# Kernel tuning notes

Hardware: AMD Instinct MI355X
Metric: run time of the kernel (lower is better)

Reference implementation:

```python
import jax, jax.numpy as jnp
import numpy as np

N = 100000          # nodes
E = 1600000         # edges (avg degree 16)
F_IN = 128          # num_node_features
H = 128             # hidden_channels
C = 8               # num_classes
EPS = 1e-5          # batchnorm eps
SLOPE = 0.01        # leaky_relu negative slope


def setup_inputs() -> dict:
    key = jax.random.key(0)
    ks = jax.random.split(key, 12)
    s = 0.05
    inp = {
        "node_feat": jax.random.normal(ks[0], (N, F_IN), jnp.float32),
        "src": jax.random.randint(ks[1], (E,), 0, N, dtype=jnp.int32),
        "dst": jax.random.randint(ks[2], (E,), 0, N, dtype=jnp.int32),
        # conv1 / conv2 (GraphConv weights + bias)
        "W1": jax.random.normal(ks[3], (F_IN, H), jnp.float32) * s,
        "b1": jnp.zeros((H,), jnp.float32),
        "W2": jax.random.normal(ks[4], (H, H), jnp.float32) * s,
        "b2": jnp.zeros((H,), jnp.float32),
        # batchnorm affine params
        "gamma1": jnp.ones((H,), jnp.float32),
        "beta1": jnp.zeros((H,), jnp.float32),
        "gamma2": jnp.ones((H,), jnp.float32),
        "beta2": jnp.zeros((H,), jnp.float32),
        # convnode1 / convnode2
        "Wn1": jax.random.normal(ks[5], (H, H), jnp.float32) * s,
        "bn1": jnp.zeros((H,), jnp.float32),
        "Wn2": jax.random.normal(ks[6], (H, H), jnp.float32) * s,
        "bn2": jnp.zeros((H,), jnp.float32),
        # node classifier
        "Wc": jax.random.normal(ks[7], (H, C), jnp.float32) * s,
        "bc": jnp.zeros((C,), jnp.float32),
    }
    return inp


def _deg_inv_sqrt(idx):
    # clamp(deg, min=1) ** -0.5, as in DGL GraphConv norm='both'
    deg = jax.ops.segment_sum(jnp.ones((E,), jnp.float32), idx, num_segments=N)
    return jnp.clip(deg, 1.0, None) ** -0.5


def _gconv(x, src, dst, W, b, out_norm, in_norm):
    # DGL GraphConv, norm='both': gather src-normalized feats, scatter-add to dst,
    # normalize by in-degree, then dense transform.
    msg = (x * out_norm[:, None])[src]                    # [E, d] gather
    agg = jax.ops.segment_sum(msg, dst, num_segments=N)   # [N, d] scatter-add
    return (agg * in_norm[:, None]) @ W + b


def _bn(x, gamma, beta):
    # training-mode BatchNorm1d: batch mean / biased var
    mean = jnp.mean(x, axis=0)
    var = jnp.var(x, axis=0)
    return (x - mean) * jax.lax.rsqrt(var + EPS) * gamma + beta


def _lrelu(x):
    return jnp.where(x >= 0, x, SLOPE * x)


def reference(node_feat, src, dst, W1, b1, W2, b2, gamma1, beta1, gamma2, beta2,
              Wn1, bn1, Wn2, bn2, Wc, bc):
    out_norm = _deg_inv_sqrt(src)   # src out-degree norm
    in_norm = _deg_inv_sqrt(dst)    # dst in-degree norm

    h = _gconv(node_feat, src, dst, W1, b1, out_norm, in_norm)
    h = _lrelu(_bn(h, gamma1, beta1))
    h = _gconv(h, src, dst, W2, b2, out_norm, in_norm)
    h = _lrelu(_bn(h, gamma2, beta2))

    hn = _lrelu(_gconv(h, src, dst, Wn1, bn1, out_norm, in_norm))
    hn = _lrelu(_gconv(hn, src, dst, Wn2, bn2, out_norm, in_norm))

    return hn @ Wc + bc   # [N, C]
```

## Files before the change

kernel.cpp:

```cpp
#include <hip/hip_runtime.h>
#include <math.h>

#define HN 128
#define NC 8
#define EPSV 1e-5f
#define SLOPEV 0.01f

typedef __attribute__((ext_vector_type(4))) float f32x4;
typedef __attribute__((ext_vector_type(8))) short bf16x8;

__device__ __forceinline__ uint bf16rne(float f) {
    uint u = __float_as_uint(f);
    return (u + 0x7fffu + ((u >> 16) & 1u)) >> 16;
}

__global__ __launch_bounds__(256) void rank_kernel(
        const int* __restrict__ src, const int* __restrict__ dst,
        int* __restrict__ degO, int* __restrict__ cntI,
        int* __restrict__ rnk, int E) {
    int base = blockIdx.x * 1024 + threadIdx.x;
    int s[4], d[4], r[4];
    #pragma unroll
    for (int k = 0; k < 4; k++) {
        int e = base + k * 256;
        if (e < E) { s[k] = src[e]; d[k] = dst[e]; }
    }
    #pragma unroll
    for (int k = 0; k < 4; k++) {
        int e = base + k * 256;
        if (e < E) atomicAdd(&degO[s[k]], 1);
    }
    #pragma unroll
    for (int k = 0; k < 4; k++) {
        int e = base + k * 256;
        if (e < E) r[k] = atomicAdd(&cntI[d[k]], 1);
    }
    #pragma unroll
    for (int k = 0; k < 4; k++) {
        int e = base + k * 256;
        if (e < E) rnk[e] = r[k];
    }
}

__global__ __launch_bounds__(256) void scan_partial(const int* __restrict__ degI,
                                                    int* __restrict__ blockSums, int n) {
    __shared__ int sS[256];
    int tid = threadIdx.x;
    int base = blockIdx.x * 1024 + tid * 4;
    int s = 0;
    #pragma unroll
    for (int j = 0; j < 4; j++) {
        int idx = base + j;
        s += (idx < n) ? degI[idx] : 0;
    }
    sS[tid] = s;
    __syncthreads();
    for (int off = 128; off; off >>= 1) {
        if (tid < off) sS[tid] += sS[tid + off];
        __syncthreads();
    }
    if (tid == 0) blockSums[blockIdx.x] = sS[0];
}

__global__ __launch_bounds__(1024) void scan_blocksums(int* __restrict__ blockSums, int nb) {
    __shared__ int sS[1024];
    int tid = threadIdx.x;
    int v = (tid < nb) ? blockSums[tid] : 0;
    sS[tid] = v;
    __syncthreads();
    for (int off = 1; off < 1024; off <<= 1) {
        int t = (tid >= off) ? sS[tid - off] : 0;
        __syncthreads();
        sS[tid] += t;
        __syncthreads();
    }
    if (tid < nb) blockSums[tid] = sS[tid] - v;
}

__global__ __launch_bounds__(256) void scan_final(const int* __restrict__ degI,
                                                  const int* __restrict__ degO,
                                                  const int* __restrict__ blockSums,
                                                  int* __restrict__ row_ptr,
                                                  float* __restrict__ onorm,
                                                  float* __restrict__ inorm, int n, int E) {
    __shared__ int sS[256];
    int tid = threadIdx.x;
    int base = blockIdx.x * 1024 + tid * 4;
    int v[4];
    int tot = 0;
    #pragma unroll
    for (int j = 0; j < 4; j++) {
        int idx = base + j;
        int vv = (idx < n) ? degI[idx] : 0;
        v[j] = tot;
        tot += vv;
    }
    sS[tid] = tot;
    __syncthreads();
    for (int off = 1; off < 256; off <<= 1) {
        int t = (tid >= off) ? sS[tid - off] : 0;
        __syncthreads();
        sS[tid] += t;
        __syncthreads();
    }
    int tb = blockSums[blockIdx.x] + sS[tid] - tot;
    #pragma unroll
    for (int j = 0; j < 4; j++) {
        int idx = base + j;
        if (idx < n) {
            row_ptr[idx] = tb + v[j];
            float a = (float)degO[idx]; if (a < 1.f) a = 1.f;
            float b = (float)degI[idx]; if (b < 1.f) b = 1.f;
            onorm[idx] = rsqrtf(a);
            inorm[idx] = rsqrtf(b);
        }
    }
    if (blockIdx.x == 0 && tid == 0) row_ptr[n] = E;
}

__global__ __launch_bounds__(256) void scatter_kernel(
        const int* __restrict__ src, const int* __restrict__ dst,
        const int* __restrict__ rnk, const int* __restrict__ row_ptr,
        int* __restrict__ srcs, int E) {
    int base = blockIdx.x * 1024 + threadIdx.x;
    int s[4], d[4], r[4], rp[4];
    #pragma unroll
    for (int k = 0; k < 4; k++) {
        int e = base + k * 256;
        if (e < E) { d[k] = dst[e]; r[k] = rnk[e]; s[k] = src[e]; }
    }
    #pragma unroll
    for (int k = 0; k < 4; k++) {
        int e = base + k * 256;
        if (e < E) rp[k] = row_ptr[d[k]];
    }
    #pragma unroll
    for (int k = 0; k < 4; k++) {
        int e = base + k * 256;
        if (e < E) srcs[rp[k] + r[k]] = s[k];
    }
}

__global__ __launch_bounds__(256) void wprep_kernel(
        const float* __restrict__ W1, const float* __restrict__ W2,
        const float* __restrict__ W3, const float* __restrict__ W4,
        ushort* __restrict__ WTh, ushort* __restrict__ WTl) {
    int i = blockIdx.x * blockDim.x + threadIdx.x;
    int l = i >> 14, r = i & 16383;
    int k = r >> 7, nn = r & 127;
    const float* W = (l == 0) ? W1 : (l == 1) ? W2 : (l == 2) ? W3 : W4;
    float w = W[k * HN + nn];
    uint hi = bf16rne(w);
    float fhi = __uint_as_float(hi << 16);
    uint lo = bf16rne(w - fhi);
    WTh[(size_t)l * 16384 + nn * HN + k] = (ushort)hi;
    WTl[(size_t)l * 16384 + nn * HN + k] = (ushort)lo;
}

__global__ __launch_bounds__(256) void pack_kernel(
        const float* __restrict__ in, const float* __restrict__ onorm,
        ushort* __restrict__ out, int total4) {
    int i = blockIdx.x * blockDim.x + threadIdx.x;
    if (i >= total4) return;
    float w = onorm[i >> 5];
    float4 v = ((const float4*)in)[i];
    ushort4 o = make_ushort4((ushort)bf16rne(v.x * w), (ushort)bf16rne(v.y * w),
                             (ushort)bf16rne(v.z * w), (ushort)bf16rne(v.w * w));
    *(ushort4*)(out + (size_t)i * 4) = o;
}

__global__ __launch_bounds__(256) void bnpack_kernel(
        const float* __restrict__ in, ushort* __restrict__ out,
        const float* __restrict__ scale, const float* __restrict__ shift,
        const float* __restrict__ onorm, int total4) {
    int i = blockIdx.x * blockDim.x + threadIdx.x;
    if (i >= total4) return;
    int cp = (i & 31) << 2;
    float w = onorm[i >> 5];
    float4 v = ((const float4*)in)[i];
    float4 s = *(const float4*)(scale + cp);
    float4 t = *(const float4*)(shift + cp);
    float h0 = fmaf(v.x, s.x, t.x); h0 = (h0 >= 0.f) ? h0 : SLOPEV * h0;
    float h1 = fmaf(v.y, s.y, t.y); h1 = (h1 >= 0.f) ? h1 : SLOPEV * h1;
    float h2 = fmaf(v.z, s.z, t.z); h2 = (h2 >= 0.f) ? h2 : SLOPEV * h2;
    float h3 = fmaf(v.w, s.w, t.w); h3 = (h3 >= 0.f) ? h3 : SLOPEV * h3;
    ushort4 o = make_ushort4((ushort)bf16rne(h0 * w), (ushort)bf16rne(h1 * w),
                             (ushort)bf16rne(h2 * w), (ushort)bf16rne(h3 * w));
    *(ushort4*)(out + (size_t)i * 4) = o;
}

__global__ __launch_bounds__(256) void agg_kernel(
        const uint* __restrict__ xb, uint* __restrict__ out,
        const int* __restrict__ srcs, const int* __restrict__ row_ptr,
        const float* __restrict__ inorm, int n) {
    int node = blockIdx.x * 4 + (threadIdx.x >> 6);
    if (node >= n) return;
    int lane = threadIdx.x & 63;
    int rp0 = row_ptr[node], rp1 = row_ptr[node + 1];
    float accx = 0.f, accy = 0.f;
    int j = rp0;
    for (; j + 3 < rp1; j += 4) {
        int s0 = srcs[j], s1 = srcs[j + 1], s2 = srcs[j + 2], s3 = srcs[j + 3];
        uint u0 = xb[(size_t)s0 * 64 + lane];
        uint u1 = xb[(size_t)s1 * 64 + lane];
        uint u2 = xb[(size_t)s2 * 64 + lane];
        uint u3 = xb[(size_t)s3 * 64 + lane];
        accx += __uint_as_float(u0 << 16) + __uint_as_float(u1 << 16)
              + __uint_as_float(u2 << 16) + __uint_as_float(u3 << 16);
        accy += __uint_as_float(u0 & 0xffff0000u) + __uint_as_float(u1 & 0xffff0000u)
              + __uint_as_float(u2 & 0xffff0000u) + __uint_as_float(u3 & 0xffff0000u);
    }
    for (; j < rp1; j++) {
        uint u0 = xb[(size_t)srcs[j] * 64 + lane];
        accx += __uint_as_float(u0 << 16);
        accy += __uint_as_float(u0 & 0xffff0000u);
    }
    float wi = inorm[node];
    uint o = bf16rne(accx * wi) | (bf16rne(accy * wi) << 16);
    out[(size_t)node * 64 + lane] = o;
}

template<int DO_STATS, int DO_LRELU, int DO_PACK>
__global__ __launch_bounds__(512) void gemm_mfma(
        const ushort* __restrict__ A, const uint4* __restrict__ WTh4,
        const uint4* __restrict__ WTl4, const float* __restrict__ bias,
        void* __restrict__ outv, float* __restrict__ colsum, float* __restrict__ colsq,
        const float* __restrict__ onorm, int n) {
    __shared__ uint4 sW[4096];
    int tid = threadIdx.x;
    #pragma unroll
    for (int it = 0; it < 4; it++) {
        int j = it * 512 + tid;
        int nrow = j >> 4, c = j & 15;
        int sidx = nrow * 16 + (c ^ (nrow & 15));
        sW[sidx] = WTh4[j];
        sW[2048 + sidx] = WTl4[j];
    }
    __syncthreads();

    int wave = tid >> 6, lane = tid & 63;
    int l15 = lane & 15, quad = lane >> 4;
    int rbase = blockIdx.x * 128 + wave * 16;
    int arow = rbase + l15; if (arow > n - 1) arow = n - 1;

    bf16x8 af[4];
    #pragma unroll
    for (int kc = 0; kc < 4; kc++)
        af[kc] = *(const bf16x8*)(A + (size_t)arow * HN + kc * 32 + quad * 8);

    f32x4 acc[8];
    #pragma unroll
    for (int t = 0; t < 8; t++) acc[t] = (f32x4){0.f, 0.f, 0.f, 0.f};

    #pragma unroll
    for (int t = 0; t < 8; t++) {
        int nn = t * 16 + l15;
        int base = nn * 16, sw = nn & 15;
        #pragma unroll
        for (int kc = 0; kc < 4; kc++) {
            int c = kc * 4 + quad;
            bf16x8 bh = *(const bf16x8*)&sW[base + (c ^ sw)];
            acc[t] = __builtin_amdgcn_mfma_f32_16x16x32_bf16(af[kc], bh, acc[t], 0, 0, 0);
        }
        #pragma unroll
        for (int kc = 0; kc < 4; kc++) {
            int c = kc * 4 + quad;
            bf16x8 bl = *(const bf16x8*)&sW[2048 + base + (c ^ sw)];
            acc[t] = __builtin_amdgcn_mfma_f32_16x16x32_bf16(af[kc], bl, acc[t], 0, 0, 0);
        }
    }

    float sarr[8], qarr[8];
    #pragma unroll
    for (int t = 0; t < 8; t++) {
        int col = t * 16 + l15;
        float bv = bias[col];
        float s = 0.f, q = 0.f;
        #pragma unroll
        for (int i = 0; i < 4; i++) {
            int row = rbase + quad * 4 + i;
            float v = acc[t][i] + bv;
            if (DO_LRELU) v = (v >= 0.f) ? v : SLOPEV * v;
            if (row < n) {
                if (DO_PACK) {
                    ((ushort*)outv)[(size_t)row * HN + col] = (ushort)bf16rne(v * onorm[row]);
                } else {
                    ((float*)outv)[(size_t)row * HN + col] = v;
                }
                if (DO_STATS) { s += v; q += v * v; }
            }
        }
        if (DO_STATS) {
            s += __shfl_xor(s, 16); q += __shfl_xor(q, 16);
            s += __shfl_xor(s, 32); q += __shfl_xor(q, 32);
        }
        sarr[t] = s; qarr[t] = q;
    }

    if (DO_STATS) {
        __syncthreads();
        float* sSum = (float*)sW;
        float* sSq  = (float*)sW + 1024;
        if (quad == 0) {
            #pragma unroll
            for (int t = 0; t < 8; t++) {
                sSum[wave * 128 + t * 16 + l15] = sarr[t];
                sSq [wave * 128 + t * 16 + l15] = qarr[t];
            }
        }
        __syncthreads();
        if (tid < 128) {
            float s = 0.f, q = 0.f;
            #pragma unroll
            for (int w = 0; w < 8; w++) { s += sSum[w * 128 + tid]; q += sSq[w * 128 + tid]; }
            atomicAdd(&colsum[tid], s);
            atomicAdd(&colsq[tid], q);
        }
    }
}

__global__ void bn_finalize(const float* __restrict__ colsum, const float* __restrict__ colsq,
                            const float* __restrict__ gamma, const float* __restrict__ beta,
                            float* __restrict__ scale, float* __restrict__ shift, int n) {
    int c = threadIdx.x;
    if (c < HN) {
        float inv = 1.f / (float)n;
        float mean = colsum[c] * inv;
        float var = colsq[c] * inv - mean * mean;
        if (var < 0.f) var = 0.f;
        float s = gamma[c] * rsqrtf(var + EPSV);
        scale[c] = s;
        shift[c] = beta[c] - mean * s;
    }
}

__global__ __launch_bounds__(256) void classifier_kernel(
        const float* __restrict__ A, const float* __restrict__ Wc,
        const float* __restrict__ bc, float* __restrict__ out, int n) {
    __shared__ float sW[HN * NC];
    __shared__ float sA[32 * 132];
    int tid = threadIdx.x;
    for (int i = tid; i < HN * NC; i += 256) sW[i] = Wc[i];
    int row0 = blockIdx.x * 32;
    for (int i = tid; i < 32 * 32; i += 256) {
        int r = i >> 5, c4 = (i & 31) << 2;
        float4 v = (row0 + r < n) ? *(const float4*)(A + (size_t)(row0 + r) * HN + c4)
                                  : make_float4(0.f, 0.f, 0.f, 0.f);
        *(float4*)&sA[r * 132 + c4] = v;
    }
    __syncthreads();
    int r = tid >> 3, c = tid & 7;
    float acc = 0.f;
    #pragma unroll 8
    for (int k = 0; k < HN; k++) acc = fmaf(sA[r * 132 + k], sW[k * NC + c], acc);
    int row = row0 + r;
    if (row < n) out[(size_t)row * NC + c] = acc + bc[c];
}

extern "C" void kernel_launch(void* const* d_in, const int* in_sizes, int n_in,
                              void* d_out, int out_size, void* d_ws, size_t ws_size,
                              hipStream_t stream) {
    const float* node_feat = (const float*)d_in[0];
    const int*   src    = (const int*)d_in[1];
    const int*   dst    = (const int*)d_in[2];
    const float* W1     = (const float*)d_in[3];
    const float* b1     = (const float*)d_in[4];
    const float* W2     = (const float*)d_in[5];
    const float* b2     = (const float*)d_in[6];
    const float* gamma1 = (const float*)d_in[7];
    const float* beta1  = (const float*)d_in[8];
    const float* gamma2 = (const float*)d_in[9];
    const float* beta2  = (const float*)d_in[10];
    const float* Wn1    = (const float*)d_in[11];
    const float* bn1    = (const float*)d_in[12];
    const float* Wn2    = (const float*)d_in[13];
    const float* bn2    = (const float*)d_in[14];
    const float* Wc     = (const float*)d_in[15];
    const float* bc     = (const float*)d_in[16];
    float* out = (float*)d_out;

    const int N = in_sizes[0] / HN;
    const int E = in_sizes[1];

    char* p = (char*)d_ws;
    float* bufA  = (float*)p; p += (size_t)N * HN * 4;
    float* bufB  = (float*)p; p += (size_t)N * HN * 4;
    float* onorm = (float*)p; p += (size_t)N * 4;
    float* inorm = (float*)p; p += (size_t)N * 4;
    float* scale = (float*)p; p += HN * 4;
    float* shift = (float*)p; p += HN * 4;
    char* zbase = p;
    float* cs1 = (float*)p; p += HN * 4;
    float* cq1 = (float*)p; p += HN * 4;
    float* cs2 = (float*)p; p += HN * 4;
    float* cq2 = (float*)p; p += HN * 4;
    int* degO = (int*)p; p += (size_t)N * 4;
    int* cntI = (int*)p; p += (size_t)N * 4;
    size_t zbytes = (size_t)(p - zbase);
    int* row_ptr = (int*)p; p += (size_t)(N + 4) * 4;
    int* blockSums = (int*)p; p += 1024 * 4;
    int* rnk     = (int*)p; p += (size_t)E * 4;
    int* srcs    = (int*)p; p += (size_t)E * 4;
    ushort* WTh  = (ushort*)p; p += 4 * 16384 * 2;
    ushort* WTl  = (ushort*)p; p += 4 * 16384 * 2;
    if ((size_t)(p - (char*)d_ws) > ws_size) return;

    hipMemsetAsync(zbase, 0, zbytes, stream);

    int gE4 = (E + 1023) / 1024;
    int nb = (N + 1023) / 1024;
    rank_kernel<<<gE4, 256, 0, stream>>>(src, dst, degO, cntI, rnk, E);
    scan_partial<<<nb, 256, 0, stream>>>(cntI, blockSums, N);
    scan_blocksums<<<1, 1024, 0, stream>>>(blockSums, nb);
    scan_final<<<nb, 256, 0, stream>>>(cntI, degO, blockSums, row_ptr, onorm, inorm, N, E);
    scatter_kernel<<<gE4, 256, 0, stream>>>(src, dst, rnk, row_ptr, srcs, E);
    wprep_kernel<<<256, 256, 0, stream>>>(W1, W2, Wn1, Wn2, WTh, WTl);

    int gAgg = (N + 3) / 4;
    int gGemm = (N + 127) / 128;
    int gApply = (N * 32 + 255) / 256;

    ushort* HbA = (ushort*)bufA;
    ushort* Abf = (ushort*)bufA + (size_t)N * HN;
    ushort* HbB = (ushort*)bufB;

    pack_kernel<<<gApply, 256, 0, stream>>>(node_feat, onorm, HbA, N * 32);
    agg_kernel<<<gAgg, 256, 0, stream>>>((const uint*)HbA, (uint*)Abf, srcs, row_ptr, inorm, N);
    gemm_mfma<1, 0, 0><<<gGemm, 512, 0, stream>>>(Abf, (const uint4*)WTh, (const uint4*)WTl,
                                                  b1, bufB, cs1, cq1, nullptr, N);
    bn_finalize<<<1, 128, 0, stream>>>(cs1, cq1, gamma1, beta1, scale, shift, N);
    bnpack_kernel<<<gApply, 256, 0, stream>>>(bufB, HbA, scale, shift, onorm, N * 32);

    agg_kernel<<<gAgg, 256, 0, stream>>>((const uint*)HbA, (uint*)Abf, srcs, row_ptr, inorm, N);
    gemm_mfma<1, 0, 0><<<gGemm, 512, 0, stream>>>(Abf, (const uint4*)(WTh + 16384),
                                                  (const uint4*)(WTl + 16384),
                                                  b2, bufB, cs2, cq2, nullptr, N);
    bn_finalize<<<1, 128, 0, stream>>>(cs2, cq2, gamma2, beta2, scale, shift, N);
    bnpack_kernel<<<gApply, 256, 0, stream>>>(bufB, HbA, scale, shift, onorm, N * 32);

    agg_kernel<<<gAgg, 256, 0, stream>>>((const uint*)HbA, (uint*)Abf, srcs, row_ptr, inorm, N);
    gemm_mfma<0, 1, 1><<<gGemm, 512, 0, stream>>>(Abf, (const uint4*)(WTh + 2 * 16384),
                                                  (const uint4*)(WTl + 2 * 16384),
                                                  bn1, HbB, nullptr, nullptr, onorm, N);

    agg_kernel<<<gAgg, 256, 0, stream>>>((const uint*)HbB, (uint*)Abf, srcs, row_ptr, inorm, N);
    gemm_mfma<0, 1, 0><<<gGemm, 512, 0, stream>>>(Abf, (const uint4*)(WTh + 3 * 16384),
                                                  (const uint4*)(WTl + 3 * 16384),
                                                  bn2, bufB, nullptr, nullptr, nullptr, N);
    classifier_kernel<<<(N + 31) / 32, 256, 0, stream>>>(bufB, Wc, bc, out, N);
}
```

Measured before the change: 757.6 us.

## Split bf16 feature buffers into four column slabs for cache-local aggregation

Feature buffers are stored as four 32-column slabs ([4][N][32] bf16) instead of row-major [N][128]. The aggregation kernel handles one slab per block range, and each wave processes four edges in parallel (16 lanes per edge), then combines the partial sums with cross-lane shuffles. Each slab is about 6.4 MB, so the random gathers for one slab should stay resident in L2/infinity cache instead of streaming the full 25.6 MB table. The cost is four passes over the CSR index arrays, 64-byte gathers in place of 256-byte row reads, and extra shuffle reductions; the GEMM A-load and the packed output store are adapted to the new layout.

```diff
diff --git a/kernel.cpp b/kernel.cpp
--- a/kernel.cpp
+++ b/kernel.cpp
@@ -159,65 +159,76 @@
 
 __global__ __launch_bounds__(256) void pack_kernel(
         const float* __restrict__ in, const float* __restrict__ onorm,
-        ushort* __restrict__ out, int total4) {
+        ushort* __restrict__ out, int nrows) {
     int i = blockIdx.x * blockDim.x + threadIdx.x;
-    if (i >= total4) return;
-    float w = onorm[i >> 5];
+    if (i >= nrows * 32) return;
+    int row = i >> 5, c4 = (i & 31) << 2;
+    float w = onorm[row];
     float4 v = ((const float4*)in)[i];
     ushort4 o = make_ushort4((ushort)bf16rne(v.x * w), (ushort)bf16rne(v.y * w),
                              (ushort)bf16rne(v.z * w), (ushort)bf16rne(v.w * w));
-    *(ushort4*)(out + (size_t)i * 4) = o;
+    int q = c4 >> 5, lc = c4 & 31;
+    *(ushort4*)(out + ((size_t)q * nrows + row) * 32 + lc) = o;
 }
 
 __global__ __launch_bounds__(256) void bnpack_kernel(
         const float* __restrict__ in, ushort* __restrict__ out,
         const float* __restrict__ scale, const float* __restrict__ shift,
-        const float* __restrict__ onorm, int total4) {
+        const float* __restrict__ onorm, int nrows) {
     int i = blockIdx.x * blockDim.x + threadIdx.x;
-    if (i >= total4) return;
-    int cp = (i & 31) << 2;
-    float w = onorm[i >> 5];
+    if (i >= nrows * 32) return;
+    int row = i >> 5, c4 = (i & 31) << 2;
+    float w = onorm[row];
     float4 v = ((const float4*)in)[i];
-    float4 s = *(const float4*)(scale + cp);
-    float4 t = *(const float4*)(shift + cp);
+    float4 s = *(const float4*)(scale + c4);
+    float4 t = *(const float4*)(shift + c4);
     float h0 = fmaf(v.x, s.x, t.x); h0 = (h0 >= 0.f) ? h0 : SLOPEV * h0;
     float h1 = fmaf(v.y, s.y, t.y); h1 = (h1 >= 0.f) ? h1 : SLOPEV * h1;
     float h2 = fmaf(v.z, s.z, t.z); h2 = (h2 >= 0.f) ? h2 : SLOPEV * h2;
     float h3 = fmaf(v.w, s.w, t.w); h3 = (h3 >= 0.f) ? h3 : SLOPEV * h3;
     ushort4 o = make_ushort4((ushort)bf16rne(h0 * w), (ushort)bf16rne(h1 * w),
                              (ushort)bf16rne(h2 * w), (ushort)bf16rne(h3 * w));
-    *(ushort4*)(out + (size_t)i * 4) = o;
+    int q = c4 >> 5, lc = c4 & 31;
+    *(ushort4*)(out + ((size_t)q * nrows + row) * 32 + lc) = o;
 }
 
 __global__ __launch_bounds__(256) void agg_kernel(
-        const uint* __restrict__ xb, uint* __restrict__ out,
+        const uint* __restrict__ xb, uint* __restrict__ outb,
         const int* __restrict__ srcs, const int* __restrict__ row_ptr,
-        const float* __restrict__ inorm, int n) {
-    int node = blockIdx.x * 4 + (threadIdx.x >> 6);
+        const float* __restrict__ inorm, int n, int nodeBlocks) {
+    int q = blockIdx.x / nodeBlocks;
+    int nb = blockIdx.x - q * nodeBlocks;
+    int node = nb * 4 + (threadIdx.x >> 6);
     if (node >= n) return;
     int lane = threadIdx.x & 63;
+    int g = lane >> 4, li = lane & 15;
+    const uint* Q = xb + (size_t)q * n * 16;
     int rp0 = row_ptr[node], rp1 = row_ptr[node + 1];
     float accx = 0.f, accy = 0.f;
-    int j = rp0;
-    for (; j + 3 < rp1; j += 4) {
-        int s0 = srcs[j], s1 = srcs[j + 1], s2 = srcs[j + 2], s3 = srcs[j + 3];
-        uint u0 = xb[(size_t)s0 * 64 + lane];
-        uint u1 = xb[(size_t)s1 * 64 + lane];
-        uint u2 = xb[(size_t)s2 * 64 + lane];
-        uint u3 = xb[(size_t)s3 * 64 + lane];
+    int j = rp0 + g;
+    for (; j + 12 < rp1; j += 16) {
+        int s0 = srcs[j], s1 = srcs[j + 4], s2 = srcs[j + 8], s3 = srcs[j + 12];
+        uint u0 = Q[(size_t)s0 * 16 + li];
+        uint u1 = Q[(size_t)s1 * 16 + li];
+        uint u2 = Q[(size_t)s2 * 16 + li];
+        uint u3 = Q[(size_t)s3 * 16 + li];
         accx += __uint_as_float(u0 << 16) + __uint_as_float(u1 << 16)
               + __uint_as_float(u2 << 16) + __uint_as_float(u3 << 16);
         accy += __uint_as_float(u0 & 0xffff0000u) + __uint_as_float(u1 & 0xffff0000u)
               + __uint_as_float(u2 & 0xffff0000u) + __uint_as_float(u3 & 0xffff0000u);
     }
-    for (; j < rp1; j++) {
-        uint u0 = xb[(size_t)srcs[j] * 64 + lane];
+    for (; j < rp1; j += 4) {
+        uint u0 = Q[(size_t)srcs[j] * 16 + li];
         accx += __uint_as_float(u0 << 16);
         accy += __uint_as_float(u0 & 0xffff0000u);
     }
-    float wi = inorm[node];
-    uint o = bf16rne(accx * wi) | (bf16rne(accy * wi) << 16);
-    out[(size_t)node * 64 + lane] = o;
+    accx += __shfl_xor(accx, 16); accy += __shfl_xor(accy, 16);
+    accx += __shfl_xor(accx, 32); accy += __shfl_xor(accy, 32);
+    if (g == 0) {
+        float wi = inorm[node];
+        uint o = bf16rne(accx * wi) | (bf16rne(accy * wi) << 16);
+        outb[((size_t)q * n + node) * 16 + li] = o;
+    }
 }
 
 template<int DO_STATS, int DO_LRELU, int DO_PACK>
@@ -246,7 +257,7 @@
     bf16x8 af[4];
     #pragma unroll
     for (int kc = 0; kc < 4; kc++)
-        af[kc] = *(const bf16x8*)(A + (size_t)arow * HN + kc * 32 + quad * 8);
+        af[kc] = *(const bf16x8*)(A + ((size_t)kc * n + arow) * 32 + quad * 8);
 
     f32x4 acc[8];
     #pragma unroll
@@ -283,7 +294,8 @@
             if (DO_LRELU) v = (v >= 0.f) ? v : SLOPEV * v;
             if (row < n) {
                 if (DO_PACK) {
-                    ((ushort*)outv)[(size_t)row * HN + col] = (ushort)bf16rne(v * onorm[row]);
+                    int qq = col >> 5, lc = col & 31;
+                    ((ushort*)outv)[((size_t)qq * n + row) * 32 + lc] = (ushort)bf16rne(v * onorm[row]);
                 } else {
                     ((float*)outv)[(size_t)row * HN + col] = v;
                 }
@@ -416,7 +428,8 @@
     scatter_kernel<<<gE4, 256, 0, stream>>>(src, dst, rnk, row_ptr, srcs, E);
     wprep_kernel<<<256, 256, 0, stream>>>(W1, W2, Wn1, Wn2, WTh, WTl);
 
-    int gAgg = (N + 3) / 4;
+    int nodeBlocks = (N + 3) / 4;
+    int gAgg = nodeBlocks * 4;
     int gGemm = (N + 127) / 128;
     int gApply = (N * 32 + 255) / 256;
 
@@ -424,26 +437,26 @@
     ushort* Abf = (ushort*)bufA + (size_t)N * HN;
     ushort* HbB = (ushort*)bufB;
 
-    pack_kernel<<<gApply, 256, 0, stream>>>(node_feat, onorm, HbA, N * 32);
-    agg_kernel<<<gAgg, 256, 0, stream>>>((const uint*)HbA, (uint*)Abf, srcs, row_ptr, inorm, N);
+    pack_kernel<<<gApply, 256, 0, stream>>>(node_feat, onorm, HbA, N);
+    agg_kernel<<<gAgg, 256, 0, stream>>>((const uint*)HbA, (uint*)Abf, srcs, row_ptr, inorm, N, nodeBlocks);
     gemm_mfma<1, 0, 0><<<gGemm, 512, 0, stream>>>(Abf, (const uint4*)WTh, (const uint4*)WTl,
                                                   b1, bufB, cs1, cq1, nullptr, N);
     bn_finalize<<<1, 128, 0, stream>>>(cs1, cq1, gamma1, beta1, scale, shift, N);
-    bnpack_kernel<<<gApply, 256, 0, stream>>>(bufB, HbA, scale, shift, onorm, N * 32);
-
-    agg_kernel<<<gAgg, 256, 0, stream>>>((const uint*)HbA, (uint*)Abf, srcs, row_ptr, inorm, N);
+    bnpack_kernel<<<gApply, 256, 0, stream>>>(bufB, HbA, scale, shift, onorm, N);
+
+    agg_kernel<<<gAgg, 256, 0, stream>>>((const uint*)HbA, (uint*)Abf, srcs, row_ptr, inorm, N, nodeBlocks);
     gemm_mfma<1, 0, 0><<<gGemm, 512, 0, stream>>>(Abf, (const uint4*)(WTh + 16384),
                                                   (const uint4*)(WTl + 16384),
                                                   b2, bufB, cs2, cq2, nullptr, N);
     bn_finalize<<<1, 128, 0, stream>>>(cs2, cq2, gamma2, beta2, scale, shift, N);
-    bnpack_kernel<<<gApply, 256, 0, stream>>>(bufB, HbA, scale, shift, onorm, N * 32);
-
-    agg_kernel<<<gAgg, 256, 0, stream>>>((const uint*)HbA, (uint*)Abf, srcs, row_ptr, inorm, N);
+    bnpack_kernel<<<gApply, 256, 0, stream>>>(bufB, HbA, scale, shift, onorm, N);
+
+    agg_kernel<<<gAgg, 256, 0, stream>>>((const uint*)HbA, (uint*)Abf, srcs, row_ptr, inorm, N, nodeBlocks);
     gemm_mfma<0, 1, 1><<<gGemm, 512, 0, stream>>>(Abf, (const uint4*)(WTh + 2 * 16384),
                                                   (const uint4*)(WTl + 2 * 16384),
                                                   bn1, HbB, nullptr, nullptr, onorm, N);
 
-    agg_kernel<<<gAgg, 256, 0, stream>>>((const uint*)HbB, (uint*)Abf, srcs, row_ptr, inorm, N);
+    agg_kernel<<<gAgg, 256, 0, stream>>>((const uint*)HbB, (uint*)Abf, srcs, row_ptr, inorm, N, nodeBlocks);
     gemm_mfma<0, 1, 0><<<gGemm, 512, 0, stream>>>(Abf, (const uint4*)(WTh + 3 * 16384),
                                                   (const uint4*)(WTl + 3 * 16384),
                                                   bn2, bufB, nullptr, nullptr, nullptr, N);
```

After: 1.116 ms. 1.47x slower.
